# Optimization experiments

Hardware: AMD Instinct MI355X
Metric: run time of the kernel (lower is better)

Reference implementation:

```python
import jax, jax.numpy as jnp
import numpy as np

B, S, V, D, H, DK, DFF, L = 2, 1024, 513, 512, 8, 64, 2048, 6
PAD_IDX = -1.0
EPS_GPE = 0.1

def _sinusoid_table(n_position, d_hid):
    pos = np.arange(n_position)[:, None].astype(np.float64)
    i = np.arange(d_hid)[None, :]
    angle = pos / np.power(10000.0, 2 * (i // 2) / d_hid)
    tab = np.zeros((n_position, d_hid), dtype=np.float32)
    tab[:, 0::2] = np.sin(angle[:, 0::2])
    tab[:, 1::2] = np.cos(angle[:, 1::2])
    return jnp.asarray(tab)

_POS_TABLE = _sinusoid_table(2048, D)

def _ln(x, g, b, eps=1e-6):
    m = x.mean(-1, keepdims=True)
    v = x.var(-1, keepdims=True)
    return (x - m) * jax.lax.rsqrt(v + eps) * g + b

def _mha(x_q, x_kv, wq_, wk_, wv_, wo_, mask, g, b):
    Bq, Sq, _ = x_q.shape
    Skv = x_kv.shape[1]
    q = (x_q @ wq_).reshape(Bq, Sq, H, DK).transpose(0, 2, 1, 3)
    k = (x_kv @ wk_).reshape(Bq, Skv, H, DK).transpose(0, 2, 1, 3)
    v = (x_kv @ wv_).reshape(Bq, Skv, H, DK).transpose(0, 2, 1, 3)
    scores = jnp.einsum('bhqd,bhkd->bhqk', q, k) / np.float32(np.sqrt(DK))
    scores = jnp.where(mask[:, None], scores, jnp.float32(-1e9))
    attn = jax.nn.softmax(scores, axis=-1)
    out = jnp.einsum('bhqk,bhkd->bhqd', attn, v).transpose(0, 2, 1, 3).reshape(Bq, Sq, D)
    return _ln(x_q + out @ wo_, g, b)

def _forward(dec_in, prev_dec_out, trg, adj, graph_length, gr_mask, gr_pos_enc_kernel,
             emb_w1, emb_b1, emb_w2, emb_b2, emb_w3, emb_b3, ln0_g, ln0_b,
             wq, wk, wv, wo, ln1_g, ln1_b,
             cq, ck, cv, co, ln2_g, ln2_b,
             ffn_w1, ffn_b1, ffn_w2, ffn_b2, ln3_g, ln3_b,
             p_w1, p_b1, p_w2, p_b2, p_w3, p_b3):
    # masks (n_ensemble = 1 so dec_in[:, :, 0, :] == dec_in)
    causal = jnp.tril(jnp.ones((S, S), bool))
    slf_mask = jnp.all(dec_in != PAD_IDX, -1)[:, None, :] & causal          # [B,S,S]
    enc_mask = jnp.all(prev_dec_out != PAD_IDX, -1)[:, None, :]             # [B,1,S]
    # word-embedding MLP: 513 -> 513 -> 513 -> 512
    h = jax.nn.relu(dec_in @ emb_w1 + emb_b1)
    h = jax.nn.relu(h @ emb_w2 + emb_b2)
    h = h @ emb_w3 + emb_b3                                                 # [B,S,D]
    # propagation graph positional encoding (k = 0..2, un-normalized branch)
    w = (1.0 - EPS_GPE) ** jnp.arange(gr_pos_enc_kernel.shape[1], dtype=jnp.float32)
    base = _POS_TABLE[:S]                                                   # [S,D]
    emb = jnp.einsum('k,bkst,td->bsd', w, gr_pos_enc_kernel, base) / w.sum()
    h = _ln(h + emb, ln0_g, ln0_b)
    for i in range(L):
        h = _mha(h, h, wq[i], wk[i], wv[i], wo[i], slf_mask, ln1_g[i], ln1_b[i])
        h = _mha(h, prev_dec_out, cq[i], ck[i], cv[i], co[i], enc_mask, ln2_g[i], ln2_b[i])
        f = jax.nn.relu(h @ ffn_w1[i] + ffn_b1[i]) @ ffn_w2[i] + ffn_b2[i]
        h = _ln(h + f, ln3_g[i], ln3_b[i])
    # projection head: 512 -> 513 -> 513 -> 513
    z = jax.nn.relu(h @ p_w1 + p_b1)
    z = jax.nn.relu(z @ p_w2 + p_b2)
    return z @ p_w3 + p_b3                                                  # [B,S,V]

def setup_inputs():
    key = jax.random.key(0)
    ks = jax.random.split(key, 24)
    def xavier(k, shape):
        lim = np.float32(np.sqrt(6.0 / (shape[-2] + shape[-1])))
        return jax.random.uniform(k, shape, jnp.float32, -lim, lim)
    inp = {}
    inp['dec_in'] = jax.random.uniform(ks[0], (B, S, V), jnp.float32)
    inp['prev_dec_out'] = jax.random.normal(ks[1], (B, S, D), jnp.float32)
    inp['trg'] = jnp.zeros((B, S, V), jnp.float32)
    inp['adj'] = jnp.zeros((B, S, S), jnp.float32)
    inp['graph_length'] = jnp.zeros((B, S, 10), jnp.float32)
    inp['gr_mask'] = jnp.zeros((B, 1, S, S), jnp.float32)
    gk = jax.random.uniform(ks[2], (B, 3, S, S), jnp.float32)
    inp['gr_pos_enc_kernel'] = gk / jnp.sum(gk, -1, keepdims=True)  # row-stochastic diffusion kernels
    SZ = max(V, D)  # sz_intermed = 513
    inp['emb_w1'] = xavier(ks[3], (V, SZ)); inp['emb_b1'] = jnp.zeros((SZ,))
    inp['emb_w2'] = xavier(ks[4], (SZ, SZ)); inp['emb_b2'] = jnp.zeros((SZ,))
    inp['emb_w3'] = xavier(ks[5], (SZ, D)); inp['emb_b3'] = jnp.zeros((D,))
    inp['ln0_g'] = jnp.ones((D,)); inp['ln0_b'] = jnp.zeros((D,))
    for name, ki, shp in [('wq', 6, (L, D, D)), ('wk', 7, (L, D, D)), ('wv', 8, (L, D, D)), ('wo', 9, (L, D, D)),
                          ('cq', 10, (L, D, D)), ('ck', 11, (L, D, D)), ('cv', 12, (L, D, D)), ('co', 13, (L, D, D)),
                          ('ffn_w1', 14, (L, D, DFF)), ('ffn_w2', 15, (L, DFF, D))]:
        inp[name] = xavier(ks[ki], shp)
    inp['ffn_b1'] = jnp.zeros((L, DFF)); inp['ffn_b2'] = jnp.zeros((L, D))
    inp['ln1_g'] = jnp.ones((L, D)); inp['ln1_b'] = jnp.zeros((L, D))
    inp['ln2_g'] = jnp.ones((L, D)); inp['ln2_b'] = jnp.zeros((L, D))
    inp['ln3_g'] = jnp.ones((L, D)); inp['ln3_b'] = jnp.zeros((L, D))
    inp['p_w1'] = xavier(ks[16], (D, V)); inp['p_b1'] = jnp.zeros((V,))
    inp['p_w2'] = xavier(ks[17], (V, V)); inp['p_b2'] = jnp.zeros((V,))
    inp['p_w3'] = xavier(ks[18], (V, V)); inp['p_b3'] = jnp.zeros((V,))
    return inp

def reference(dec_in, prev_dec_out, trg, adj, graph_length, gr_mask, gr_pos_enc_kernel,
              emb_w1, emb_b1, emb_w2, emb_b2, emb_w3, emb_b3, ln0_g, ln0_b,
              wq, wk, wv, wo, ln1_g, ln1_b,
              cq, ck, cv, co, ln2_g, ln2_b,
              ffn_w1, ffn_b1, ffn_w2, ffn_b2, ln3_g, ln3_b,
              p_w1, p_b1, p_w2, p_b2, p_w3, p_b3):
    return _forward(dec_in, prev_dec_out, trg, adj, graph_length, gr_mask, gr_pos_enc_kernel,
                    emb_w1, emb_b1, emb_w2, emb_b2, emb_w3, emb_b3, ln0_g, ln0_b,
                    wq, wk, wv, wo, ln1_g, ln1_b,
                    cq, ck, cv, co, ln2_g, ln2_b,
                    ffn_w1, ffn_b1, ffn_w2, ffn_b2, ln3_g, ln3_b,
                    p_w1, p_b1, p_w2, p_b2, p_w3, p_b3)
```

## Files before the change

### kernel.cpp

```cpp
#include <hip/hip_runtime.h>
#include <hip/hip_bf16.h>
#include <stdint.h>

#define BB 2
#define SS 1024
#define VV 513
#define VP 576
#define DD 512
#define HH 8
#define DKK 64
#define DFFN 2048
#define LL 6
#define MM (BB * SS)

typedef __bf16 bf16x8 __attribute__((ext_vector_type(8)));
typedef float f32x4 __attribute__((ext_vector_type(4)));
typedef unsigned short us8 __attribute__((ext_vector_type(8)));

static __device__ inline unsigned short f2bf(float f) {
  union { float f; unsigned u; } v; v.f = f;
  unsigned u = v.u;
  unsigned r = (u + 0x7FFFu + ((u >> 16) & 1u)) >> 16;
  return (unsigned short)r;
}

static __device__ inline bf16x8 ldfrag(const unsigned short* p) {
  us8 r = *(const us8*)p;
  return __builtin_bit_cast(bf16x8, r);
}

typedef __attribute__((address_space(3))) void lds_void;
typedef const __attribute__((address_space(1))) void glb_void;
static __device__ inline void gl_lds16(const void* g, void* l) {
  __builtin_amdgcn_global_load_lds((glb_void*)g, (lds_void*)l, 16, 0, 0);
}

static __device__ inline bf16x8 ldfrag_swz(const unsigned short* base, int row, int kloc) {
  const unsigned byte = (unsigned)(row * 128 + kloc * 2) ^ (unsigned)((row & 7) << 4);
  return ldfrag((const unsigned short*)((const char*)base + byte));
}

struct GemmP {
  const unsigned short* A;
  const unsigned short* B0; const unsigned short* B1; const unsigned short* B2;
  const float* bias;
  float* C;
  unsigned short* D0; unsigned short* D1; unsigned short* D2;
  int Kp, Np, ldc, Nreal, relu;
};

template<int NB>
__global__ __launch_bounds__(256)
void gemm_tpl(GemmP p)
{
  __shared__ unsigned short Al[2][64 * 64];
  __shared__ unsigned short Bl[2][64 * 64];
  const int tid = threadIdx.x;
  const int l = tid & 63, w = tid >> 6;
  const int wm = w >> 1, wn = w & 1;
  const int lr = l & 15, lg = l >> 4;

  const int nbn = p.Np >> 6;
  int sel = 0, bx = blockIdx.x;
  if (NB > 1) { sel = bx / nbn; bx -= sel * nbn; }
  const unsigned short* Bmat = p.B0;
  if (NB > 1 && sel == 1) Bmat = p.B1;
  if (NB > 2 && sel == 2) Bmat = p.B2;
  const int m0 = blockIdx.y << 6, n0 = bx << 6;

  f32x4 acc[2][2];
  const f32x4 zf = {0.f, 0.f, 0.f, 0.f};
#pragma unroll
  for (int i = 0; i < 2; ++i)
#pragma unroll
    for (int j = 0; j < 2; ++j) acc[i][j] = zf;

  const size_t Kp = (size_t)p.Kp;
  const unsigned short* Abase = p.A + (size_t)m0 * Kp;
  const unsigned short* Bbase = Bmat + (size_t)n0 * Kp;

  auto stage = [&](int buf, int kt) {
    const int k0 = kt << 6;
#pragma unroll
    for (int j = 0; j < 2; ++j) {
      const int ti = j * 256 + tid;
      const int row = ti >> 3;
      const int sinner = (ti & 7) ^ (row & 7);
      gl_lds16(Abase + (size_t)row * Kp + k0 + sinner * 8, &Al[buf][ti * 8]);
    }
#pragma unroll
    for (int j = 0; j < 2; ++j) {
      const int ti = j * 256 + tid;
      const int row = ti >> 3;
      const int sinner = (ti & 7) ^ (row & 7);
      gl_lds16(Bbase + (size_t)row * Kp + k0 + sinner * 8, &Bl[buf][ti * 8]);
    }
  };

  const int nt = p.Kp >> 6;
  int cur = 0;
  stage(0, 0);
  asm volatile("s_waitcnt vmcnt(0)" ::: "memory");
  __syncthreads();

  for (int kt = 0; kt < nt; ++kt) {
    if (kt + 1 < nt) stage(cur ^ 1, kt + 1);
#pragma unroll
    for (int ks = 0; ks < 2; ++ks) {
      bf16x8 af[2], bfv[2];
#pragma unroll
      for (int mf = 0; mf < 2; ++mf)
        af[mf] = ldfrag_swz(Al[cur], wm * 32 + mf * 16 + lr, ks * 32 + lg * 8);
#pragma unroll
      for (int nf = 0; nf < 2; ++nf)
        bfv[nf] = ldfrag_swz(Bl[cur], wn * 32 + nf * 16 + lr, ks * 32 + lg * 8);
#pragma unroll
      for (int mf = 0; mf < 2; ++mf)
#pragma unroll
        for (int nf = 0; nf < 2; ++nf)
          acc[mf][nf] = __builtin_amdgcn_mfma_f32_16x16x32_bf16(af[mf], bfv[nf], acc[mf][nf], 0, 0, 0);
    }
    if (kt + 1 < nt) {
      asm volatile("s_waitcnt vmcnt(0)" ::: "memory");
      __syncthreads();
    }
    cur ^= 1;
  }

  unsigned short* Dsel = p.D0;
  if (NB > 1 && sel == 1) Dsel = p.D1;
  if (NB > 2 && sel == 2) Dsel = p.D2;
#pragma unroll
  for (int mf = 0; mf < 2; ++mf) {
#pragma unroll
    for (int r = 0; r < 4; ++r) {
      const int grow = m0 + wm * 32 + mf * 16 + (lg << 2) + r;
#pragma unroll
      for (int nf = 0; nf < 2; ++nf) {
        const int gcol = n0 + wn * 32 + nf * 16 + lr;
        float v = acc[mf][nf][r];
        if (p.bias && gcol < p.Nreal) v += p.bias[gcol];
        if (p.relu) v = fmaxf(v, 0.f);
        if (Dsel) Dsel[(size_t)grow * p.Np + gcol] = f2bf(v);
        if (p.C && gcol < p.Nreal) p.C[(size_t)grow * p.ldc + gcol] = v;
      }
    }
  }
}

struct GemmBat {
  const unsigned short* A;
  const unsigned short* B[12];
  unsigned short* D[12];
  int Kp, Np;
};

__global__ __launch_bounds__(256)
void gemm_bat(GemmBat p)
{
  __shared__ unsigned short Al[2][64 * 64];
  __shared__ unsigned short Bl[2][64 * 64];
  const int tid = threadIdx.x;
  const int l = tid & 63, w = tid >> 6;
  const int wm = w >> 1, wn = w & 1;
  const int lr = l & 15, lg = l >> 4;

  const int nbn = p.Np >> 6;
  const int sel = blockIdx.x / nbn;
  const int bx = blockIdx.x - sel * nbn;
  const unsigned short* Bmat = p.B[sel];
  unsigned short* Dmat = p.D[sel];
  const int m0 = blockIdx.y << 6, n0 = bx << 6;

  f32x4 acc[2][2];
  const f32x4 zf = {0.f, 0.f, 0.f, 0.f};
#pragma unroll
  for (int i = 0; i < 2; ++i)
#pragma unroll
    for (int j = 0; j < 2; ++j) acc[i][j] = zf;

  const size_t Kp = (size_t)p.Kp;
  const unsigned short* Abase = p.A + (size_t)m0 * Kp;
  const unsigned short* Bbase = Bmat + (size_t)n0 * Kp;

  auto stage = [&](int buf, int kt) {
    const int k0 = kt << 6;
#pragma unroll
    for (int j = 0; j < 2; ++j) {
      const int ti = j * 256 + tid;
      const int row = ti >> 3;
      const int sinner = (ti & 7) ^ (row & 7);
      gl_lds16(Abase + (size_t)row * Kp + k0 + sinner * 8, &Al[buf][ti * 8]);
    }
#pragma unroll
    for (int j = 0; j < 2; ++j) {
      const int ti = j * 256 + tid;
      const int row = ti >> 3;
      const int sinner = (ti & 7) ^ (row & 7);
      gl_lds16(Bbase + (size_t)row * Kp + k0 + sinner * 8, &Bl[buf][ti * 8]);
    }
  };

  const int nt = p.Kp >> 6;
  int cur = 0;
  stage(0, 0);
  asm volatile("s_waitcnt vmcnt(0)" ::: "memory");
  __syncthreads();

  for (int kt = 0; kt < nt; ++kt) {
    if (kt + 1 < nt) stage(cur ^ 1, kt + 1);
#pragma unroll
    for (int ks = 0; ks < 2; ++ks) {
      bf16x8 af[2], bfv[2];
#pragma unroll
      for (int mf = 0; mf < 2; ++mf)
        af[mf] = ldfrag_swz(Al[cur], wm * 32 + mf * 16 + lr, ks * 32 + lg * 8);
#pragma unroll
      for (int nf = 0; nf < 2; ++nf)
        bfv[nf] = ldfrag_swz(Bl[cur], wn * 32 + nf * 16 + lr, ks * 32 + lg * 8);
#pragma unroll
      for (int mf = 0; mf < 2; ++mf)
#pragma unroll
        for (int nf = 0; nf < 2; ++nf)
          acc[mf][nf] = __builtin_amdgcn_mfma_f32_16x16x32_bf16(af[mf], bfv[nf], acc[mf][nf], 0, 0, 0);
    }
    if (kt + 1 < nt) {
      asm volatile("s_waitcnt vmcnt(0)" ::: "memory");
      __syncthreads();
    }
    cur ^= 1;
  }

#pragma unroll
  for (int mf = 0; mf < 2; ++mf) {
#pragma unroll
    for (int r = 0; r < 4; ++r) {
      const int grow = m0 + wm * 32 + mf * 16 + (lg << 2) + r;
#pragma unroll
      for (int nf = 0; nf < 2; ++nf) {
        const int gcol = n0 + wn * 32 + nf * 16 + lr;
        Dmat[(size_t)grow * p.Np + gcol] = f2bf(acc[mf][nf][r]);
      }
    }
  }
}

__global__ __launch_bounds__(256)
void vtrans_kernel(const unsigned short* __restrict__ src, unsigned short* __restrict__ dst)
{
  __shared__ unsigned short t[64][72];
  const int s0 = blockIdx.x << 6, h = blockIdx.y;
  const int b = blockIdx.z & 1, li = blockIdx.z >> 1;
  const unsigned short* vb = src + (size_t)li * MM * DD;
  unsigned short* vbT = dst + (size_t)li * MM * DD;
  const int tid = threadIdx.x;
  const int rr = tid >> 2, cbase = (tid & 3) * 2;
#pragma unroll
  for (int j = 0; j < 2; ++j) {
    const int ch = cbase + j;
    *(us8*)&t[rr][ch * 8] = *(const us8*)(vb + ((size_t)(b * SS) + s0 + rr) * DD + h * DKK + ch * 8);
  }
  __syncthreads();
#pragma unroll
  for (int j = 0; j < 2; ++j) {
    const int ch = cbase + j;
    us8 o;
#pragma unroll
    for (int e = 0; e < 8; ++e) o[e] = t[ch * 8 + e][rr];
    *(us8*)(vbT + (((size_t)(b * HH) + h) * DKK + rr) * SS + s0 + ch * 8) = o;
  }
}

template<int CAUSAL>
__global__ __launch_bounds__(128)
void attn_kernel(const unsigned short* __restrict__ Qb,
                 const unsigned short* __restrict__ Kb,
                 const unsigned short* __restrict__ VbT,
                 unsigned short* __restrict__ Ob,
                 const float* __restrict__ maskadd)
{
  __shared__ unsigned short Kl[2][64 * 64];
  __shared__ unsigned short Vl[2][64 * 64];
  __shared__ unsigned short Pl[2 * 16 * 72];
  const int tid = threadIdx.x;
  const int l = tid & 63, w = tid >> 6;
  const int qt = blockIdx.x, h = blockIdx.y, b = blockIdx.z;
  const int lr = l & 15, lg = l >> 4;
  const int qbase = qt * 32 + w * 16;

  bf16x8 qf[2];
  {
    const unsigned short* qrow = Qb + ((size_t)(b * SS) + qbase + lr) * DD + h * DKK;
    qf[0] = ldfrag(qrow + (lg << 3));
    qf[1] = ldfrag(qrow + 32 + (lg << 3));
  }

  const unsigned short* Kbase = Kb + (size_t)(b * SS) * DD + h * DKK;
  const unsigned short* Vbase = VbT + ((size_t)(b * HH) + h) * DKK * SS;

  auto stage = [&](int buf, int kt) {
#pragma unroll
    for (int j = 0; j < 4; ++j) {
      const int ti = j * 128 + tid;
      const int row = ti >> 3;
      const int ch = (ti & 7) ^ (row & 7);
      gl_lds16(Kbase + (size_t)(kt * 64 + row) * DD + ch * 8, &Kl[buf][ti * 8]);
    }
#pragma unroll
    for (int j = 0; j < 4; ++j) {
      const int ti = j * 128 + tid;
      const int row = ti >> 3;
      const int ch = (ti & 7) ^ (row & 7);
      gl_lds16(Vbase + (size_t)row * SS + kt * 64 + ch * 8, &Vl[buf][ti * 8]);
    }
  };

  f32x4 accO[4];
  const f32x4 zf = {0.f, 0.f, 0.f, 0.f};
#pragma unroll
  for (int i = 0; i < 4; ++i) accO[i] = zf;
  float mold[4] = {-1e30f, -1e30f, -1e30f, -1e30f};
  float lsum[4] = {0.f, 0.f, 0.f, 0.f};

  const int ktmax = CAUSAL ? ((qt >> 1) + 1) : (SS / 64);
  stage(0, 0);
  asm volatile("s_waitcnt vmcnt(0)" ::: "memory");
  __syncthreads();

  for (int kt = 0; kt < ktmax; ++kt) {
    const int cur = kt & 1;
    if (kt + 1 < ktmax) stage(cur ^ 1, kt + 1);
    float sc[4][4];
    __builtin_amdgcn_s_setprio(1);
#pragma unroll
    for (int nf = 0; nf < 4; ++nf) {
      f32x4 s = zf;
      bf16x8 k0 = ldfrag_swz(Kl[cur], nf * 16 + lr, lg * 8);
      bf16x8 k1 = ldfrag_swz(Kl[cur], nf * 16 + lr, 32 + lg * 8);
      s = __builtin_amdgcn_mfma_f32_16x16x32_bf16(qf[0], k0, s, 0, 0, 0);
      s = __builtin_amdgcn_mfma_f32_16x16x32_bf16(qf[1], k1, s, 0, 0, 0);
      const int kglob = kt * 64 + nf * 16 + lr;
      const float madd = maskadd[b * SS + kglob];
#pragma unroll
      for (int r = 0; r < 4; ++r) {
        const int qglob = qbase + (lg << 2) + r;
        sc[nf][r] = (CAUSAL && kglob > qglob) ? -1e9f : s[r] * 0.125f + madd;
      }
    }
    __builtin_amdgcn_s_setprio(0);
#pragma unroll
    for (int r = 0; r < 4; ++r) {
      float mloc = fmaxf(fmaxf(sc[0][r], sc[1][r]), fmaxf(sc[2][r], sc[3][r]));
#pragma unroll
      for (int off = 1; off < 16; off <<= 1)
        mloc = fmaxf(mloc, __shfl_xor(mloc, off, 64));
      const float mnew = fmaxf(mold[r], mloc);
      const float corr = __expf(mold[r] - mnew);
      float ps = 0.f;
#pragma unroll
      for (int nf = 0; nf < 4; ++nf) {
        const float pv = __expf(sc[nf][r] - mnew);
        sc[nf][r] = pv;
        ps += pv;
      }
#pragma unroll
      for (int off = 1; off < 16; off <<= 1)
        ps += __shfl_xor(ps, off, 64);
      lsum[r] = lsum[r] * corr + ps;
#pragma unroll
      for (int nf = 0; nf < 4; ++nf) accO[nf][r] *= corr;
      mold[r] = mnew;
    }
    unsigned short* pw = &Pl[w * 16 * 72];
#pragma unroll
    for (int nf = 0; nf < 4; ++nf)
#pragma unroll
      for (int r = 0; r < 4; ++r)
        pw[((lg << 2) + r) * 72 + nf * 16 + lr] = f2bf(sc[nf][r]);
    bf16x8 pa0 = ldfrag(&pw[lr * 72 + (lg << 3)]);
    bf16x8 pa1 = ldfrag(&pw[lr * 72 + 32 + (lg << 3)]);
    __builtin_amdgcn_s_setprio(1);
#pragma unroll
    for (int nf = 0; nf < 4; ++nf) {
      bf16x8 v0 = ldfrag_swz(Vl[cur], nf * 16 + lr, lg * 8);
      bf16x8 v1 = ldfrag_swz(Vl[cur], nf * 16 + lr, 32 + lg * 8);
      accO[nf] = __builtin_amdgcn_mfma_f32_16x16x32_bf16(pa0, v0, accO[nf], 0, 0, 0);
      accO[nf] = __builtin_amdgcn_mfma_f32_16x16x32_bf16(pa1, v1, accO[nf], 0, 0, 0);
    }
    __builtin_amdgcn_s_setprio(0);
    asm volatile("s_waitcnt vmcnt(0)" ::: "memory");
    __syncthreads();
  }
#pragma unroll
  for (int r = 0; r < 4; ++r) {
    const float inv = 1.f / lsum[r];
    const size_t orow = ((size_t)(b * SS) + qbase + (lg << 2) + r) * DD + h * DKK;
#pragma unroll
    for (int nf = 0; nf < 4; ++nf)
      Ob[orow + nf * 16 + lr] = f2bf(accO[nf][r] * inv);
  }
}

__global__ __launch_bounds__(256)
void addln_kernel(const float* __restrict__ a, const float* __restrict__ c,
                  const float* __restrict__ g, const float* __restrict__ bb,
                  float* __restrict__ hf, unsigned short* __restrict__ hb)
{
  const int row = blockIdx.x * 4 + (threadIdx.x >> 6);
  const int l = threadIdx.x & 63;
  const float* ar = a + (size_t)row * DD + l * 8;
  const float* cr = c + (size_t)row * DD + l * 8;
  f32x4 x0 = *(const f32x4*)ar + *(const f32x4*)cr;
  f32x4 x1 = *(const f32x4*)(ar + 4) + *(const f32x4*)(cr + 4);
  float sum = x0[0] + x0[1] + x0[2] + x0[3] + x1[0] + x1[1] + x1[2] + x1[3];
#pragma unroll
  for (int off = 1; off < 64; off <<= 1) sum += __shfl_xor(sum, off, 64);
  const float mean = sum * (1.f / 512.f);
  float vs = 0.f;
#pragma unroll
  for (int j = 0; j < 4; ++j) { float d0 = x0[j] - mean; float d1 = x1[j] - mean; vs += d0 * d0 + d1 * d1; }
#pragma unroll
  for (int off = 1; off < 64; off <<= 1) vs += __shfl_xor(vs, off, 64);
  const float rs = rsqrtf(vs * (1.f / 512.f) + 1e-6f);
  const f32x4 g0 = *(const f32x4*)(g + l * 8), g1 = *(const f32x4*)(g + l * 8 + 4);
  const f32x4 b0 = *(const f32x4*)(bb + l * 8), b1 = *(const f32x4*)(bb + l * 8 + 4);
  f32x4 o0, o1;
  us8 ob;
#pragma unroll
  for (int j = 0; j < 4; ++j) {
    o0[j] = (x0[j] - mean) * rs * g0[j] + b0[j];
    o1[j] = (x1[j] - mean) * rs * g1[j] + b1[j];
    ob[j] = f2bf(o0[j]); ob[j + 4] = f2bf(o1[j]);
  }
  float* of = hf + (size_t)row * DD + l * 8;
  *(f32x4*)of = o0; *(f32x4*)(of + 4) = o1;
  *(us8*)(hb + (size_t)row * DD + l * 8) = ob;
}

__global__ __launch_bounds__(64)
void rowvalid_kernel(const float* __restrict__ x, int n, float* __restrict__ out)
{
  const int row = blockIdx.x, l = threadIdx.x;
  const float* xr = x + (size_t)row * n;
  int ok = 1;
  for (int j = l; j < n; j += 64) ok &= (xr[j] != -1.0f) ? 1 : 0;
  ok = __all(ok) ? 1 : 0;
  if (l == 0) out[row] = ok ? 0.f : -1e9f;
}

__global__ void postable_kernel(unsigned short* __restrict__ tabT)
{
  const int i = blockIdx.x * blockDim.x + threadIdx.x;
  if (i >= DD * SS) return;
  const int d = i >> 10, s = i & 1023;
  const float ex = (float)(2 * (d >> 1)) * (1.0f / (float)DD);
  const float ang = (float)s * powf(10000.0f, -ex);
  tabT[i] = f2bf((d & 1) ? cosf(ang) : sinf(ang));
}

__global__ void gpec_kernel(const float* __restrict__ gk, unsigned short* __restrict__ Mb)
{
  const int i = blockIdx.x * blockDim.x + threadIdx.x;
  if (i >= BB * SS * SS) return;
  const int b = i / (SS * SS);
  const int rem = i - b * (SS * SS);
  const float* p = gk + (size_t)b * 3 * SS * SS + rem;
  Mb[i] = f2bf((p[0] + 0.9f * p[SS * SS] + 0.81f * p[2 * SS * SS]) * (1.0f / 2.71f));
}

__global__ __launch_bounds__(256)
void wconv_kernel(const float* __restrict__ W, unsigned short* __restrict__ WT,
                  int K, int N, int Kp, int Np)
{
  __shared__ float t[64][65];
  const float* Wl = W + (size_t)blockIdx.z * K * N;
  unsigned short* WTl = WT + (size_t)blockIdx.z * Np * Kp;
  const int n0 = blockIdx.x << 6, k0 = blockIdx.y << 6;
  const int tid = threadIdx.x;
  const int cx = tid & 63, ry = tid >> 6;
#pragma unroll
  for (int i = 0; i < 16; ++i) {
    const int kk = k0 + ry + i * 4, nn = n0 + cx;
    t[ry + i * 4][cx] = (kk < K && nn < N) ? Wl[(size_t)kk * N + nn] : 0.f;
  }
  __syncthreads();
#pragma unroll
  for (int i = 0; i < 16; ++i) {
    const int nn = n0 + ry + i * 4, kk = k0 + cx;
    WTl[(size_t)nn * Kp + kk] = f2bf(t[cx][ry + i * 4]);
  }
}

struct WconvB { const float* W[8]; unsigned short* WT[8]; };
__global__ __launch_bounds__(256)
void wconv8_kernel(WconvB p)
{
  __shared__ float t[64][65];
  const int z = blockIdx.z;
  const int wi = z / LL, li = z - wi * LL;
  const float* Wl = p.W[wi] + (size_t)li * DD * DD;
  unsigned short* WTl = p.WT[wi] + (size_t)li * DD * DD;
  const int n0 = blockIdx.x << 6, k0 = blockIdx.y << 6;
  const int cx = threadIdx.x & 63, ry = threadIdx.x >> 6;
#pragma unroll
  for (int i = 0; i < 16; ++i)
    t[ry + i * 4][cx] = Wl[(size_t)(k0 + ry + i * 4) * DD + n0 + cx];
  __syncthreads();
#pragma unroll
  for (int i = 0; i < 16; ++i)
    WTl[(size_t)(n0 + ry + i * 4) * DD + k0 + cx] = f2bf(t[cx][ry + i * 4]);
}

__global__ void aconv_kernel(const float* __restrict__ A, unsigned short* __restrict__ Ab,
                             int N, int Np, int total)
{
  const int i = blockIdx.x * blockDim.x + threadIdx.x;
  if (i >= total) return;
  const int row = i / Np, col = i - row * Np;
  Ab[i] = (col < N) ? f2bf(A[(size_t)row * N + col]) : (unsigned short)0;
}

static inline void g1(hipStream_t s, const unsigned short* A, const unsigned short* B,
                      const float* bias, float* C, unsigned short* D,
                      int Kp, int Np, int ldc, int Nreal, int relu)
{
  GemmP p{};
  p.A = A; p.B0 = B; p.bias = bias; p.C = C; p.D0 = D;
  p.Kp = Kp; p.Np = Np; p.ldc = ldc; p.Nreal = Nreal; p.relu = relu;
  gemm_tpl<1><<<dim3(Np >> 6, MM >> 6), 256, 0, s>>>(p);
}

static inline void g3(hipStream_t s, const unsigned short* A, const unsigned short* B0,
                      const unsigned short* B1, const unsigned short* B2,
                      unsigned short* D0, unsigned short* D1, unsigned short* D2,
                      int Kp, int Np)
{
  GemmP p{};
  p.A = A; p.B0 = B0; p.B1 = B1; p.B2 = B2; p.D0 = D0; p.D1 = D1; p.D2 = D2;
  p.Kp = Kp; p.Np = Np; p.ldc = Np; p.Nreal = Np; p.relu = 0;
  gemm_tpl<3><<<dim3(3 * (Np >> 6), MM >> 6), 256, 0, s>>>(p);
}

extern "C" void kernel_launch(void* const* d_in, const int* in_sizes, int n_in,
                              void* d_out, int out_size, void* d_ws, size_t ws_size,
                              hipStream_t stream)
{
  (void)in_sizes; (void)n_in; (void)out_size; (void)ws_size;
  const float* dec_in = (const float*)d_in[0];
  const float* prev   = (const float*)d_in[1];
  const float* gk     = (const float*)d_in[6];
  const float* emb_w1 = (const float*)d_in[7];
  const float* emb_b1 = (const float*)d_in[8];
  const float* emb_w2 = (const float*)d_in[9];
  const float* emb_b2 = (const float*)d_in[10];
  const float* emb_w3 = (const float*)d_in[11];
  const float* emb_b3 = (const float*)d_in[12];
  const float* ln0_g  = (const float*)d_in[13];
  const float* ln0_b  = (const float*)d_in[14];
  const float* wq     = (const float*)d_in[15];
  const float* wk     = (const float*)d_in[16];
  const float* wv     = (const float*)d_in[17];
  const float* wo     = (const float*)d_in[18];
  const float* cq     = (const float*)d_in[19];
  const float* ck     = (const float*)d_in[20];
  const float* cv     = (const float*)d_in[21];
  const float* co     = (const float*)d_in[22];
  const float* ffn_w1 = (const float*)d_in[23];
  const float* ffn_w2 = (const float*)d_in[24];
  const float* ffn_b1 = (const float*)d_in[25];
  const float* ffn_b2 = (const float*)d_in[26];
  const float* ln1_g  = (const float*)d_in[27];
  const float* ln1_b  = (const float*)d_in[28];
  const float* ln2_g  = (const float*)d_in[29];
  const float* ln2_b  = (const float*)d_in[30];
  const float* ln3_g  = (const float*)d_in[31];
  const float* ln3_b  = (const float*)d_in[32];
  const float* p_w1   = (const float*)d_in[33];
  const float* p_b1   = (const float*)d_in[34];
  const float* p_w2   = (const float*)d_in[35];
  const float* p_b2   = (const float*)d_in[36];
  const float* p_w3   = (const float*)d_in[37];
  const float* p_b3   = (const float*)d_in[38];

  char* wsp = (char*)d_ws;
  auto carve = [&](size_t bytes) { char* r = wsp; wsp += (bytes + 255) & ~(size_t)255; return r; };

  unsigned short* decb  = (unsigned short*)carve((size_t)MM * VP * 2);
  unsigned short* prevb = (unsigned short*)carve((size_t)MM * DD * 2);
  float*          hf    = (float*)carve((size_t)MM * DD * 4);
  unsigned short* hb    = (unsigned short*)carve((size_t)MM * DD * 2);
  float*          xf1   = (float*)carve((size_t)MM * DD * 4);
  unsigned short* tb1   = (unsigned short*)carve((size_t)MM * DFFN * 2);
  unsigned short* Mbb   = tb1;
  float*          xf2   = (float*)((char*)tb1 + (size_t)MM * SS * 2);
  unsigned short* tb2a  = (unsigned short*)carve((size_t)MM * VP * 2);
  unsigned short* tb2b  = (unsigned short*)carve((size_t)MM * VP * 2);
  unsigned short* qb    = (unsigned short*)carve((size_t)MM * DD * 2);
  unsigned short* kb    = (unsigned short*)carve((size_t)MM * DD * 2);
  unsigned short* vb    = (unsigned short*)carve((size_t)MM * DD * 2);
  unsigned short* vbT   = (unsigned short*)carve((size_t)MM * DD * 2);
  float* kvs = (float*)carve((size_t)MM * 4);
  float* kve = (float*)carve((size_t)MM * 4);
  unsigned short* postabt = (unsigned short*)carve((size_t)DD * SS * 2);
  unsigned short* ew1t  = (unsigned short*)carve((size_t)VP * VP * 2);
  unsigned short* ew2t  = (unsigned short*)carve((size_t)VP * VP * 2);
  unsigned short* ew3t  = (unsigned short*)carve((size_t)DD * VP * 2);
  unsigned short* wqt   = (unsigned short*)carve((size_t)LL * DD * DD * 2);
  unsigned short* wkt   = (unsigned short*)carve((size_t)LL * DD * DD * 2);
  unsigned short* wvt   = (unsigned short*)carve((size_t)LL * DD * DD * 2);
  unsigned short* wot   = (unsigned short*)carve((size_t)LL * DD * DD * 2);
  unsigned short* cqt   = (unsigned short*)carve((size_t)LL * DD * DD * 2);
  unsigned short* ckt   = (unsigned short*)carve((size_t)LL * DD * DD * 2);
  unsigned short* cvt   = (unsigned short*)carve((size_t)LL * DD * DD * 2);
  unsigned short* cot   = (unsigned short*)carve((size_t)LL * DD * DD * 2);
  unsigned short* f1t   = (unsigned short*)carve((size_t)LL * DFFN * DD * 2);
  unsigned short* f2t   = (unsigned short*)carve((size_t)LL * DD * DFFN * 2);
  unsigned short* p1t   = (unsigned short*)carve((size_t)VP * DD * 2);
  unsigned short* p2t   = (unsigned short*)carve((size_t)VP * VP * 2);
  unsigned short* p3t   = (unsigned short*)carve((size_t)VP * VP * 2);
  unsigned short* ckall = (unsigned short*)carve((size_t)LL * MM * DD * 2);
  unsigned short* cvall = (unsigned short*)carve((size_t)LL * MM * DD * 2);
  unsigned short* cvbT  = (unsigned short*)carve((size_t)LL * MM * DD * 2);

  const dim3 agrid(SS / 32, HH, BB);

  rowvalid_kernel<<<MM, 64, 0, stream>>>(dec_in, VV, kvs);
  rowvalid_kernel<<<MM, 64, 0, stream>>>(prev, DD, kve);
  aconv_kernel<<<(MM * VP + 255) / 256, 256, 0, stream>>>(dec_in, decb, VV, VP, MM * VP);
  aconv_kernel<<<(MM * DD + 255) / 256, 256, 0, stream>>>(prev, prevb, DD, DD, MM * DD);
  postable_kernel<<<(DD * SS + 255) / 256, 256, 0, stream>>>(postabt);
  gpec_kernel<<<(BB * SS * SS + 255) / 256, 256, 0, stream>>>(gk, Mbb);

  {
    WconvB wb{};
    wb.W[0] = wq; wb.W[1] = wk; wb.W[2] = wv; wb.W[3] = wo;
    wb.W[4] = cq; wb.W[5] = ck; wb.W[6] = cv; wb.W[7] = co;
    wb.WT[0] = wqt; wb.WT[1] = wkt; wb.WT[2] = wvt; wb.WT[3] = wot;
    wb.WT[4] = cqt; wb.WT[5] = ckt; wb.WT[6] = cvt; wb.WT[7] = cot;
    wconv8_kernel<<<dim3(8, 8, 8 * LL), 256, 0, stream>>>(wb);
  }
  wconv_kernel<<<dim3(9, 9, 1), 256, 0, stream>>>(emb_w1, ew1t, VV, VV, VP, VP);
  wconv_kernel<<<dim3(9, 9, 1), 256, 0, stream>>>(emb_w2, ew2t, VV, VV, VP, VP);
  wconv_kernel<<<dim3(8, 9, 1), 256, 0, stream>>>(emb_w3, ew3t, VV, DD, VP, DD);
  wconv_kernel<<<dim3(32, 8, LL), 256, 0, stream>>>(ffn_w1, f1t, DD, DFFN, DD, DFFN);
  wconv_kernel<<<dim3(8, 32, LL), 256, 0, stream>>>(ffn_w2, f2t, DFFN, DD, DFFN, DD);
  wconv_kernel<<<dim3(9, 8, 1), 256, 0, stream>>>(p_w1, p1t, DD, VV, DD, VP);
  wconv_kernel<<<dim3(9, 9, 1), 256, 0, stream>>>(p_w2, p2t, VV, VV, VP, VP);
  wconv_kernel<<<dim3(9, 9, 1), 256, 0, stream>>>(p_w3, p3t, VV, VV, VP, VP);

  {
    GemmBat p{};
    p.A = prevb; p.Kp = DD; p.Np = DD;
    for (int i = 0; i < LL; ++i) {
      p.B[2 * i]     = ckt + (size_t)i * DD * DD;
      p.B[2 * i + 1] = cvt + (size_t)i * DD * DD;
      p.D[2 * i]     = ckall + (size_t)i * MM * DD;
      p.D[2 * i + 1] = cvall + (size_t)i * MM * DD;
    }
    gemm_bat<<<dim3(12 * (DD >> 6), MM >> 6), 256, 0, stream>>>(p);
    vtrans_kernel<<<dim3(16, 8, 2 * LL), 256, 0, stream>>>(cvall, cvbT);
  }

  g1(stream, decb, ew1t, emb_b1, nullptr, tb2a, VP, VP, VP, VV, 1);
  g1(stream, tb2a, ew2t, emb_b2, nullptr, tb2b, VP, VP, VP, VV, 1);
  g1(stream, tb2b, ew3t, emb_b3, xf1, nullptr, VP, DD, DD, DD, 0);
  g1(stream, Mbb, postabt, nullptr, xf2, nullptr, SS, DD, DD, DD, 0);
  addln_kernel<<<MM / 4, 256, 0, stream>>>(xf1, xf2, ln0_g, ln0_b, hf, hb);

  for (int i = 0; i < LL; ++i) {
    const size_t od = (size_t)i * DD * DD;
    g3(stream, hb, wqt + od, wkt + od, wvt + od, qb, kb, vb, DD, DD);
    vtrans_kernel<<<dim3(16, 8, 2), 256, 0, stream>>>(vb, vbT);
    attn_kernel<1><<<agrid, 128, 0, stream>>>(qb, kb, vbT, qb, kvs);
    g1(stream, qb, wot + od, nullptr, xf1, nullptr, DD, DD, DD, DD, 0);
    addln_kernel<<<MM / 4, 256, 0, stream>>>(hf, xf1, ln1_g + i * DD, ln1_b + i * DD, hf, hb);
    g1(stream, hb, cqt + od, nullptr, nullptr, qb, DD, DD, DD, DD, 0);
    attn_kernel<0><<<agrid, 128, 0, stream>>>(qb, ckall + (size_t)i * MM * DD,
                                              cvbT + (size_t)i * MM * DD, qb, kve);
    g1(stream, qb, cot + od, nullptr, xf1, nullptr, DD, DD, DD, DD, 0);
    addln_kernel<<<MM / 4, 256, 0, stream>>>(hf, xf1, ln2_g + i * DD, ln2_b + i * DD, hf, hb);
    g1(stream, hb, f1t + (size_t)i * DFFN * DD, ffn_b1 + i * DFFN, nullptr, tb1, DD, DFFN, DFFN, DFFN, 1);
    g1(stream, tb1, f2t + (size_t)i * DD * DFFN, ffn_b2 + i * DD, xf1, nullptr, DFFN, DD, DD, DD, 0);
    addln_kernel<<<MM / 4, 256, 0, stream>>>(hf, xf1, ln3_g + i * DD, ln3_b + i * DD, hf, hb);
  }

  g1(stream, hb, p1t, p_b1, nullptr, tb2a, DD, VP, VP, VV, 1);
  g1(stream, tb2a, p2t, p_b2, nullptr, tb2b, VP, VP, VP, VV, 1);
  g1(stream, tb2b, p3t, p_b3, (float*)d_out, nullptr, VP, VP, VV, VV, 0);
}
```

Before: 1.169 ms.

## Triple-buffer LDS staging in GEMM and attention, widen FFN1 tile to 128

Moves the GEMM, batched GEMM and attention kernels from a double-buffered to a triple-buffered LDS pipeline. Each iteration does a partial vmcnt wait plus one barrier, and prefetches two tiles ahead instead of draining all loads and syncing twice. Adds a 128-wide N tile variant for the FFN up-projection to reuse each A tile across more columns, and swaps powf for exp2f in the positional table. This costs extra LDS per block, which may lower occupancy. The hand-tuned vmcnt counts must match the number of loads issued per stage.

```diff
diff --git a/kernel.cpp b/kernel.cpp
--- a/kernel.cpp
+++ b/kernel.cpp
@@ -40,6 +40,8 @@
   return ldfrag((const unsigned short*)((const char*)base + byte));
 }
 
+static __device__ inline int rot3(int x) { return (x == 2) ? 0 : x + 1; }
+
 struct GemmP {
   const unsigned short* A;
   const unsigned short* B0; const unsigned short* B1; const unsigned short* B2;
@@ -49,31 +51,32 @@
   int Kp, Np, ldc, Nreal, relu;
 };
 
-template<int NB>
+template<int NB, int NT>
 __global__ __launch_bounds__(256)
 void gemm_tpl(GemmP p)
 {
-  __shared__ unsigned short Al[2][64 * 64];
-  __shared__ unsigned short Bl[2][64 * 64];
+  constexpr int FN = NT / 32;
+  __shared__ unsigned short Al[3][64 * 64];
+  __shared__ unsigned short Bl[3][NT * 64];
   const int tid = threadIdx.x;
   const int l = tid & 63, w = tid >> 6;
   const int wm = w >> 1, wn = w & 1;
   const int lr = l & 15, lg = l >> 4;
 
-  const int nbn = p.Np >> 6;
+  const int nbn = p.Np / NT;
   int sel = 0, bx = blockIdx.x;
   if (NB > 1) { sel = bx / nbn; bx -= sel * nbn; }
   const unsigned short* Bmat = p.B0;
   if (NB > 1 && sel == 1) Bmat = p.B1;
   if (NB > 2 && sel == 2) Bmat = p.B2;
-  const int m0 = blockIdx.y << 6, n0 = bx << 6;
-
-  f32x4 acc[2][2];
+  const int m0 = blockIdx.y << 6, n0 = bx * NT;
+
+  f32x4 acc[2][FN];
   const f32x4 zf = {0.f, 0.f, 0.f, 0.f};
 #pragma unroll
   for (int i = 0; i < 2; ++i)
 #pragma unroll
-    for (int j = 0; j < 2; ++j) acc[i][j] = zf;
+    for (int j = 0; j < FN; ++j) acc[i][j] = zf;
 
   const size_t Kp = (size_t)p.Kp;
   const unsigned short* Abase = p.A + (size_t)m0 * Kp;
@@ -85,46 +88,48 @@
     for (int j = 0; j < 2; ++j) {
       const int ti = j * 256 + tid;
       const int row = ti >> 3;
-      const int sinner = (ti & 7) ^ (row & 7);
-      gl_lds16(Abase + (size_t)row * Kp + k0 + sinner * 8, &Al[buf][ti * 8]);
-    }
-#pragma unroll
-    for (int j = 0; j < 2; ++j) {
+      const int ch = (ti & 7) ^ (row & 7);
+      gl_lds16(Abase + (size_t)row * Kp + k0 + ch * 8, &Al[buf][ti * 8]);
+    }
+#pragma unroll
+    for (int j = 0; j < FN; ++j) {
       const int ti = j * 256 + tid;
       const int row = ti >> 3;
-      const int sinner = (ti & 7) ^ (row & 7);
-      gl_lds16(Bbase + (size_t)row * Kp + k0 + sinner * 8, &Bl[buf][ti * 8]);
+      const int ch = (ti & 7) ^ (row & 7);
+      gl_lds16(Bbase + (size_t)row * Kp + k0 + ch * 8, &Bl[buf][ti * 8]);
     }
   };
 
   const int nt = p.Kp >> 6;
-  int cur = 0;
   stage(0, 0);
-  asm volatile("s_waitcnt vmcnt(0)" ::: "memory");
-  __syncthreads();
+  if (nt > 1) stage(1, 1);
+  int cb = 0, sb = 2;
 
   for (int kt = 0; kt < nt; ++kt) {
-    if (kt + 1 < nt) stage(cur ^ 1, kt + 1);
+    if (kt + 1 < nt) {
+      if constexpr (FN == 2) asm volatile("s_waitcnt vmcnt(4)" ::: "memory");
+      else                   asm volatile("s_waitcnt vmcnt(6)" ::: "memory");
+    } else {
+      asm volatile("s_waitcnt vmcnt(0)" ::: "memory");
+    }
+    __builtin_amdgcn_s_barrier();
+    if (kt + 2 < nt) { stage(sb, kt + 2); sb = rot3(sb); }
 #pragma unroll
     for (int ks = 0; ks < 2; ++ks) {
-      bf16x8 af[2], bfv[2];
+      bf16x8 af[2], bfv[FN];
 #pragma unroll
       for (int mf = 0; mf < 2; ++mf)
-        af[mf] = ldfrag_swz(Al[cur], wm * 32 + mf * 16 + lr, ks * 32 + lg * 8);
-#pragma unroll
-      for (int nf = 0; nf < 2; ++nf)
-        bfv[nf] = ldfrag_swz(Bl[cur], wn * 32 + nf * 16 + lr, ks * 32 + lg * 8);
+        af[mf] = ldfrag_swz(Al[cb], wm * 32 + mf * 16 + lr, ks * 32 + lg * 8);
+#pragma unroll
+      for (int nf = 0; nf < FN; ++nf)
+        bfv[nf] = ldfrag_swz(Bl[cb], wn * (NT / 2) + nf * 16 + lr, ks * 32 + lg * 8);
 #pragma unroll
       for (int mf = 0; mf < 2; ++mf)
 #pragma unroll
-        for (int nf = 0; nf < 2; ++nf)
+        for (int nf = 0; nf < FN; ++nf)
           acc[mf][nf] = __builtin_amdgcn_mfma_f32_16x16x32_bf16(af[mf], bfv[nf], acc[mf][nf], 0, 0, 0);
     }
-    if (kt + 1 < nt) {
-      asm volatile("s_waitcnt vmcnt(0)" ::: "memory");
-      __syncthreads();
-    }
-    cur ^= 1;
+    cb = rot3(cb);
   }
 
   unsigned short* Dsel = p.D0;
@@ -136,8 +141,8 @@
     for (int r = 0; r < 4; ++r) {
       const int grow = m0 + wm * 32 + mf * 16 + (lg << 2) + r;
 #pragma unroll
-      for (int nf = 0; nf < 2; ++nf) {
-        const int gcol = n0 + wn * 32 + nf * 16 + lr;
+      for (int nf = 0; nf < FN; ++nf) {
+        const int gcol = n0 + wn * (NT / 2) + nf * 16 + lr;
         float v = acc[mf][nf][r];
         if (p.bias && gcol < p.Nreal) v += p.bias[gcol];
         if (p.relu) v = fmaxf(v, 0.f);
@@ -158,8 +163,8 @@
 __global__ __launch_bounds__(256)
 void gemm_bat(GemmBat p)
 {
-  __shared__ unsigned short Al[2][64 * 64];
-  __shared__ unsigned short Bl[2][64 * 64];
+  __shared__ unsigned short Al[3][64 * 64];
+  __shared__ unsigned short Bl[3][64 * 64];
   const int tid = threadIdx.x;
   const int l = tid & 63, w = tid >> 6;
   const int wm = w >> 1, wn = w & 1;
@@ -189,46 +194,44 @@
     for (int j = 0; j < 2; ++j) {
       const int ti = j * 256 + tid;
       const int row = ti >> 3;
-      const int sinner = (ti & 7) ^ (row & 7);
-      gl_lds16(Abase + (size_t)row * Kp + k0 + sinner * 8, &Al[buf][ti * 8]);
+      const int ch = (ti & 7) ^ (row & 7);
+      gl_lds16(Abase + (size_t)row * Kp + k0 + ch * 8, &Al[buf][ti * 8]);
     }
 #pragma unroll
     for (int j = 0; j < 2; ++j) {
       const int ti = j * 256 + tid;
       const int row = ti >> 3;
-      const int sinner = (ti & 7) ^ (row & 7);
-      gl_lds16(Bbase + (size_t)row * Kp + k0 + sinner * 8, &Bl[buf][ti * 8]);
+      const int ch = (ti & 7) ^ (row & 7);
+      gl_lds16(Bbase + (size_t)row * Kp + k0 + ch * 8, &Bl[buf][ti * 8]);
     }
   };
 
   const int nt = p.Kp >> 6;
-  int cur = 0;
   stage(0, 0);
-  asm volatile("s_waitcnt vmcnt(0)" ::: "memory");
-  __syncthreads();
+  if (nt > 1) stage(1, 1);
+  int cb = 0, sb = 2;
 
   for (int kt = 0; kt < nt; ++kt) {
-    if (kt + 1 < nt) stage(cur ^ 1, kt + 1);
+    if (kt + 1 < nt) asm volatile("s_waitcnt vmcnt(4)" ::: "memory");
+    else             asm volatile("s_waitcnt vmcnt(0)" ::: "memory");
+    __builtin_amdgcn_s_barrier();
+    if (kt + 2 < nt) { stage(sb, kt + 2); sb = rot3(sb); }
 #pragma unroll
     for (int ks = 0; ks < 2; ++ks) {
       bf16x8 af[2], bfv[2];
 #pragma unroll
       for (int mf = 0; mf < 2; ++mf)
-        af[mf] = ldfrag_swz(Al[cur], wm * 32 + mf * 16 + lr, ks * 32 + lg * 8);
+        af[mf] = ldfrag_swz(Al[cb], wm * 32 + mf * 16 + lr, ks * 32 + lg * 8);
 #pragma unroll
       for (int nf = 0; nf < 2; ++nf)
-        bfv[nf] = ldfrag_swz(Bl[cur], wn * 32 + nf * 16 + lr, ks * 32 + lg * 8);
+        bfv[nf] = ldfrag_swz(Bl[cb], wn * 32 + nf * 16 + lr, ks * 32 + lg * 8);
 #pragma unroll
       for (int mf = 0; mf < 2; ++mf)
 #pragma unroll
         for (int nf = 0; nf < 2; ++nf)
           acc[mf][nf] = __builtin_amdgcn_mfma_f32_16x16x32_bf16(af[mf], bfv[nf], acc[mf][nf], 0, 0, 0);
     }
-    if (kt + 1 < nt) {
-      asm volatile("s_waitcnt vmcnt(0)" ::: "memory");
-      __syncthreads();
-    }
-    cur ^= 1;
+    cb = rot3(cb);
   }
 
 #pragma unroll
@@ -279,8 +282,8 @@
                  unsigned short* __restrict__ Ob,
                  const float* __restrict__ maskadd)
 {
-  __shared__ unsigned short Kl[2][64 * 64];
-  __shared__ unsigned short Vl[2][64 * 64];
+  __shared__ unsigned short Kl[3][64 * 64];
+  __shared__ unsigned short Vl[3][64 * 64];
   __shared__ unsigned short Pl[2 * 16 * 72];
   const int tid = threadIdx.x;
   const int l = tid & 63, w = tid >> 6;
@@ -324,19 +327,21 @@
 
   const int ktmax = CAUSAL ? ((qt >> 1) + 1) : (SS / 64);
   stage(0, 0);
-  asm volatile("s_waitcnt vmcnt(0)" ::: "memory");
-  __syncthreads();
+  if (ktmax > 1) stage(1, 1);
+  int cb = 0, sb = 2;
 
   for (int kt = 0; kt < ktmax; ++kt) {
-    const int cur = kt & 1;
-    if (kt + 1 < ktmax) stage(cur ^ 1, kt + 1);
+    if (kt + 1 < ktmax) asm volatile("s_waitcnt vmcnt(8)" ::: "memory");
+    else                asm volatile("s_waitcnt vmcnt(0)" ::: "memory");
+    __builtin_amdgcn_s_barrier();
+    if (kt + 2 < ktmax) { stage(sb, kt + 2); sb = rot3(sb); }
     float sc[4][4];
     __builtin_amdgcn_s_setprio(1);
 #pragma unroll
     for (int nf = 0; nf < 4; ++nf) {
       f32x4 s = zf;
-      bf16x8 k0 = ldfrag_swz(Kl[cur], nf * 16 + lr, lg * 8);
-      bf16x8 k1 = ldfrag_swz(Kl[cur], nf * 16 + lr, 32 + lg * 8);
+      bf16x8 k0 = ldfrag_swz(Kl[cb], nf * 16 + lr, lg * 8);
+      bf16x8 k1 = ldfrag_swz(Kl[cb], nf * 16 + lr, 32 + lg * 8);
       s = __builtin_amdgcn_mfma_f32_16x16x32_bf16(qf[0], k0, s, 0, 0, 0);
       s = __builtin_amdgcn_mfma_f32_16x16x32_bf16(qf[1], k1, s, 0, 0, 0);
       const int kglob = kt * 64 + nf * 16 + lr;
@@ -382,14 +387,13 @@
     __builtin_amdgcn_s_setprio(1);
 #pragma unroll
     for (int nf = 0; nf < 4; ++nf) {
-      bf16x8 v0 = ldfrag_swz(Vl[cur], nf * 16 + lr, lg * 8);
-      bf16x8 v1 = ldfrag_swz(Vl[cur], nf * 16 + lr, 32 + lg * 8);
+      bf16x8 v0 = ldfrag_swz(Vl[cb], nf * 16 + lr, lg * 8);
+      bf16x8 v1 = ldfrag_swz(Vl[cb], nf * 16 + lr, 32 + lg * 8);
       accO[nf] = __builtin_amdgcn_mfma_f32_16x16x32_bf16(pa0, v0, accO[nf], 0, 0, 0);
       accO[nf] = __builtin_amdgcn_mfma_f32_16x16x32_bf16(pa1, v1, accO[nf], 0, 0, 0);
     }
     __builtin_amdgcn_s_setprio(0);
-    asm volatile("s_waitcnt vmcnt(0)" ::: "memory");
-    __syncthreads();
+    cb = rot3(cb);
   }
 #pragma unroll
   for (int r = 0; r < 4; ++r) {
@@ -454,7 +458,7 @@
   if (i >= DD * SS) return;
   const int d = i >> 10, s = i & 1023;
   const float ex = (float)(2 * (d >> 1)) * (1.0f / (float)DD);
-  const float ang = (float)s * powf(10000.0f, -ex);
+  const float ang = (float)s * exp2f(ex * -13.287712379549449f);
   tabT[i] = f2bf((d & 1) ? cosf(ang) : sinf(ang));
 }
 
@@ -527,7 +531,16 @@
   GemmP p{};
   p.A = A; p.B0 = B; p.bias = bias; p.C = C; p.D0 = D;
   p.Kp = Kp; p.Np = Np; p.ldc = ldc; p.Nreal = Nreal; p.relu = relu;
-  gemm_tpl<1><<<dim3(Np >> 6, MM >> 6), 256, 0, s>>>(p);
+  gemm_tpl<1, 64><<<dim3(Np >> 6, MM >> 6), 256, 0, s>>>(p);
+}
+
+static inline void g1w(hipStream_t s, const unsigned short* A, const unsigned short* B,
+                       const float* bias, unsigned short* D, int Kp, int Np, int relu)
+{
+  GemmP p{};
+  p.A = A; p.B0 = B; p.bias = bias; p.D0 = D;
+  p.Kp = Kp; p.Np = Np; p.ldc = Np; p.Nreal = Np; p.relu = relu;
+  gemm_tpl<1, 128><<<dim3(Np >> 7, MM >> 6), 256, 0, s>>>(p);
 }
 
 static inline void g3(hipStream_t s, const unsigned short* A, const unsigned short* B0,
@@ -538,7 +551,7 @@
   GemmP p{};
   p.A = A; p.B0 = B0; p.B1 = B1; p.B2 = B2; p.D0 = D0; p.D1 = D1; p.D2 = D2;
   p.Kp = Kp; p.Np = Np; p.ldc = Np; p.Nreal = Np; p.relu = 0;
-  gemm_tpl<3><<<dim3(3 * (Np >> 6), MM >> 6), 256, 0, s>>>(p);
+  gemm_tpl<3, 64><<<dim3(3 * (Np >> 6), MM >> 6), 256, 0, s>>>(p);
 }
 
 extern "C" void kernel_launch(void* const* d_in, const int* in_sizes, int n_in,
@@ -679,7 +692,7 @@
                                               cvbT + (size_t)i * MM * DD, qb, kve);
     g1(stream, qb, cot + od, nullptr, xf1, nullptr, DD, DD, DD, DD, 0);
     addln_kernel<<<MM / 4, 256, 0, stream>>>(hf, xf1, ln2_g + i * DD, ln2_b + i * DD, hf, hb);
-    g1(stream, hb, f1t + (size_t)i * DFFN * DD, ffn_b1 + i * DFFN, nullptr, tb1, DD, DFFN, DFFN, DFFN, 1);
+    g1w(stream, hb, f1t + (size_t)i * DFFN * DD, ffn_b1 + i * DFFN, tb1, DD, DFFN, 1);
     g1(stream, tb1, f2t + (size_t)i * DD * DFFN, ffn_b2 + i * DD, xf1, nullptr, DFFN, DD, DD, DD, 0);
     addln_kernel<<<MM / 4, 256, 0, stream>>>(hf, xf1, ln3_g + i * DD, ln3_b + i * DD, hf, hb);
   }
```

Result: no change. 1.172 ms (+0.2%).
